# Performance work log

Measured on AMD Instinct MI355X. Metric: run time of the kernel, lower is better.

Reference implementation:

```python
import jax, jax.numpy as jnp
import numpy as np


def _conv2d_valid(x, w):
    # x: (N, C, H, W), w: (O, C, kH, kW) -> (N, O, H-kH+1, W-kW+1)
    return jax.lax.conv_general_dilated(
        x, w, window_strides=(1, 1), padding='VALID',
        dimension_numbers=('NCHW', 'OIHW', 'NCHW'))


def setup_inputs() -> dict:
    key = jax.random.key(0)
    kx, ky = jax.random.split(key)
    x = jax.random.normal(kx, (16, 64, 128, 128), dtype=jnp.float32)
    y = jax.random.normal(ky, (64, 64, 16, 16), dtype=jnp.float32)
    return {"x": x, "y": y}


def reference(x, y):
    # Normalize each of the K kernels to unit L2 norm (sum over C, kH, kW).
    normed_y = y / jnp.sqrt(jnp.sum(y * y, axis=(1, 2, 3), keepdims=True))
    # Per-window L2 norm of x via ones-kernel box conv over x^2.
    ones_kernel = jnp.ones(y.shape, dtype=x.dtype)
    x_norm = jnp.sqrt(_conv2d_valid(x * x, ones_kernel))
    # Normalized cross-correlation, clamped at zero.
    diss = _conv2d_valid(x, normed_y) / x_norm
    return jax.nn.relu(diss)
```

## Files before the change

kernel.cpp:

```cpp
#include <hip/hip_runtime.h>
#include <stdint.h>

#define GAS __attribute__((address_space(1)))
#define LAS __attribute__((address_space(3)))

typedef __attribute__((ext_vector_type(8))) short short8;
typedef __attribute__((ext_vector_type(4))) float float4v;
typedef __attribute__((ext_vector_type(4))) unsigned int uint4v;

__device__ __forceinline__ unsigned short f2bf(float f) {
  union { float f; unsigned int u; } v; v.f = f;
  unsigned int r = v.u + 0x7fffu + ((v.u >> 16) & 1u);
  return (unsigned short)(r >> 16);
}

__device__ __forceinline__ void async_g2l16(const void* g, void* l) {
  __builtin_amdgcn_global_load_lds((const GAS unsigned int*)g,
                                   (LAS unsigned int*)l, 16, 0, 0);
}

__global__ void knorm_y(const float* __restrict__ y, unsigned short* __restrict__ y_t) {
  int o = blockIdx.x;
  int tid = threadIdx.x;
  const float* yo = y + o * 16384;
  float s = 0.f;
  for (int idx = tid; idx < 16384; idx += 256) { float v = yo[idx]; s += v * v; }
  for (int off = 32; off; off >>= 1) s += __shfl_down(s, off, 64);
  __shared__ float red[4];
  if ((tid & 63) == 0) red[tid >> 6] = s;
  __syncthreads();
  float rn = 1.0f / sqrtf(red[0] + red[1] + red[2] + red[3]);
  for (int idx = tid; idx < 16384; idx += 256) {
    int c = idx >> 8, dy = (idx >> 4) & 15, dx = idx & 15;
    unsigned short b = f2bf(yo[idx] * rn);
    int dst = ((dy * 16 + dx) * 64 + o) * 64 + (((c >> 3) ^ (o & 7)) << 3) + (c & 7);
    y_t[dst] = b;
  }
}

__global__ void ktrans_x(const float* __restrict__ x, unsigned short* __restrict__ x_t,
                         float* __restrict__ s) {
  int h = blockIdx.x, n = blockIdx.y;
  int tid = threadIdx.x;
  __shared__ __align__(16) unsigned short tb[8192];
  __shared__ float sb[256];
  const float* xb = x + ((size_t)n * 64) * 16384 + h * 128;
  for (int idx = tid; idx < 8192; idx += 256) {
    int c = idx >> 7, w = idx & 127;
    float v = xb[(size_t)c * 16384 + w];
    tb[w * 64 + (((c >> 3) ^ (w & 7)) << 3) + (c & 7)] = f2bf(v);
  }
  int w = tid & 127, half = tid >> 7;
  float acc = 0.f;
  for (int c = half * 32; c < half * 32 + 32; ++c) {
    float v = xb[(size_t)c * 16384 + w];
    acc += v * v;
  }
  sb[tid] = acc;
  __syncthreads();
  uint4v* dst = (uint4v*)(x_t + ((size_t)(n * 128 + h)) * 8192);
  const uint4v* src = (const uint4v*)tb;
  for (int idx = tid; idx < 1024; idx += 256) dst[idx] = src[idx];
  if (tid < 128) s[((size_t)(n * 128 + h)) * 128 + tid] = sb[tid] + sb[tid + 128];
}

__global__ void knorm_x(const float* __restrict__ s, float* __restrict__ invn) {
  int idx = blockIdx.x * 256 + threadIdx.x;
  if (idx >= 16 * 113 * 113) return;
  int n = idx / 12769, r = idx % 12769;
  int i = r / 113, j = r % 113;
  const float* sp = s + ((size_t)n * 128 + i) * 128 + j;
  float acc = 0.f;
#pragma unroll
  for (int dy = 0; dy < 16; ++dy) {
    float rowacc = 0.f;
#pragma unroll
    for (int dx = 0; dx < 16; ++dx) rowacc += sp[dy * 128 + dx];
    acc += rowacc;
  }
  invn[idx] = 1.0f / sqrtf(acc);
}

__launch_bounds__(256, 2)
__global__ void kconv(const unsigned short* __restrict__ x_t,
                      const unsigned short* __restrict__ y_t,
                      const float* __restrict__ invn,
                      float* __restrict__ out) {
  int i = blockIdx.x;
  int n = blockIdx.y;
  int tid = threadIdx.x;
  int lane = tid & 63, wave = tid >> 6;
  int lane15 = lane & 15, q = lane >> 4;
  int wrow = wave >> 1, wcol = wave & 1;

  __shared__ __align__(16) char smem[49152];
  char* const A0 = smem;
  char* const A1 = smem + 16384;
  char* const B0 = smem + 32768;
  char* const B1 = smem + 40960;

  const char* xrow0 = (const char*)(x_t + ((size_t)(n * 128 + i)) * 8192);

  auto stageA = [&](int dy, char* buf) {
    const char* src = xrow0 + (size_t)dy * 16384;
#pragma unroll
    for (int it = 0; it < 4; ++it) {
      int chunk = it * 256 + wave * 64;
      async_g2l16(src + (chunk + lane) * 16, buf + chunk * 16);
    }
  };
  auto stageB = [&](int t, char* buf) {
    const char* src = (const char*)(y_t + (size_t)t * 4096);
#pragma unroll
    for (int it = 0; it < 2; ++it) {
      int chunk = it * 256 + wave * 64;
      async_g2l16(src + (chunk + lane) * 16, buf + chunk * 16);
    }
  };

  float4v acc[4][2];
#pragma unroll
  for (int mt = 0; mt < 4; ++mt)
#pragma unroll
    for (int nt = 0; nt < 2; ++nt) acc[mt][nt] = (float4v){0.f, 0.f, 0.f, 0.f};

  int boff[2][2];
#pragma unroll
  for (int nt = 0; nt < 2; ++nt)
#pragma unroll
    for (int cb = 0; cb < 2; ++cb) {
      int o = wcol * 32 + nt * 16 + lane15;
      boff[nt][cb] = o * 128 + (((q + cb * 4) ^ (o & 7)) << 4);
    }
  int abase[4];
#pragma unroll
  for (int mt = 0; mt < 4; ++mt) abase[mt] = (wrow * 64 + mt * 16 + lane15) * 128;

  stageB(0, B0);
  stageA(0, A0);
  __syncthreads();

#pragma unroll 1
  for (int t = 0; t < 256; ++t) {
    int dx = t & 15, dy = t >> 4;
    if (t < 255) {
      stageB(t + 1, (t & 1) ? B0 : B1);
      if (((t + 1) & 15) == 0) stageA((t + 1) >> 4, ((((t + 1) >> 4) & 1) ? A1 : A0));
    }
    char* Ab = (dy & 1) ? A1 : A0;
    char* Bb = (t & 1) ? B1 : B0;

    short8 bf[2][2];
#pragma unroll
    for (int nt = 0; nt < 2; ++nt)
#pragma unroll
      for (int cb = 0; cb < 2; ++cb) bf[nt][cb] = *(const short8*)(Bb + boff[nt][cb]);

    int xr = (lane15 + dx) & 7;
#pragma unroll
    for (int cb = 0; cb < 2; ++cb) {
      int aoff = dx * 128 + ((((q + cb * 4) ^ xr)) << 4);
#pragma unroll
      for (int mt = 0; mt < 4; ++mt) {
        short8 a = *(const short8*)(Ab + abase[mt] + aoff);
        acc[mt][0] = __builtin_amdgcn_mfma_f32_16x16x32_bf16(a, bf[0][cb], acc[mt][0], 0, 0, 0);
        acc[mt][1] = __builtin_amdgcn_mfma_f32_16x16x32_bf16(a, bf[1][cb], acc[mt][1], 0, 0, 0);
      }
    }
    __syncthreads();
  }

  float* cs = (float*)smem;
#pragma unroll
  for (int mt = 0; mt < 4; ++mt)
#pragma unroll
    for (int nt = 0; nt < 2; ++nt) {
      int o = wcol * 32 + nt * 16 + lane15;
      int j0 = wrow * 64 + mt * 16 + q * 4;
      *(float4v*)(cs + o * 132 + j0) = acc[mt][nt];
    }
  __syncthreads();
  const float* ivp = invn + ((size_t)n * 113 + i) * 113;
  float* op = out + (size_t)n * 64 * 12769 + (size_t)i * 113;
  for (int idx = tid; idx < 8192; idx += 256) {
    int o = idx >> 7, j = idx & 127;
    if (j < 113) {
      float v = cs[o * 132 + j] * ivp[j];
      op[(size_t)o * 12769 + j] = fmaxf(v, 0.f);
    }
  }
}

extern "C" void kernel_launch(void* const* d_in, const int* in_sizes, int n_in,
                              void* d_out, int out_size, void* d_ws, size_t ws_size,
                              hipStream_t stream) {
  const float* x = (const float*)d_in[0];
  const float* y = (const float*)d_in[1];
  float* out = (float*)d_out;
  char* ws = (char*)d_ws;
  unsigned short* x_t = (unsigned short*)ws;
  unsigned short* y_t = (unsigned short*)(ws + 33554432);
  float* s = (float*)(ws + 35651584);
  float* invn = (float*)(ws + 36700160);

  hipLaunchKernelGGL(knorm_y, dim3(64), dim3(256), 0, stream, y, y_t);
  hipLaunchKernelGGL(ktrans_x, dim3(128, 16), dim3(256), 0, stream, x, x_t, s);
  hipLaunchKernelGGL(knorm_x, dim3(799), dim3(256), 0, stream, s, invn);
  hipLaunchKernelGGL(kconv, dim3(113, 16), dim3(256), 0, stream, x_t, y_t, invn, out);
}
```

Before: 598.8 us.

## Load conv filter fragments directly to registers, drop B LDS staging

The filter tensor is re-laid out so each lane can load its MFMA B fragments straight from global memory into registers. This removes the per-tap LDS staging and the barrier after every tap, leaving one barrier per filter row. LDS use drops to 32KB, so occupancy rises to 3 blocks per CU, and the epilogue is split into two halves to fit. The x transpose is fused with the sum-of-squares pass, and the window norm becomes a separable box sum. The cost is more global/L2 traffic for the filter, with one register double buffer hiding its latency.

```diff
diff --git a/kernel.cpp b/kernel.cpp
--- a/kernel.cpp
+++ b/kernel.cpp
@@ -19,7 +19,11 @@
                                    (LAS unsigned int*)l, 16, 0, 0);
 }
 
-__global__ void knorm_y(const float* __restrict__ y, unsigned short* __restrict__ y_t) {
+__device__ __forceinline__ void vmem_drain() {
+  asm volatile("s_waitcnt vmcnt(0)" ::: "memory");
+}
+
+__global__ void knorm_y(const float* __restrict__ y, unsigned short* __restrict__ y_t2) {
   int o = blockIdx.x;
   int tid = threadIdx.x;
   const float* yo = y + o * 16384;
@@ -30,11 +34,13 @@
   if ((tid & 63) == 0) red[tid >> 6] = s;
   __syncthreads();
   float rn = 1.0f / sqrtf(red[0] + red[1] + red[2] + red[3]);
+  int og = o >> 4, ol = o & 15;
   for (int idx = tid; idx < 16384; idx += 256) {
     int c = idx >> 8, dy = (idx >> 4) & 15, dx = idx & 15;
-    unsigned short b = f2bf(yo[idx] * rn);
-    int dst = ((dy * 16 + dx) * 64 + o) * 64 + (((c >> 3) ^ (o & 7)) << 3) + (c & 7);
-    y_t[dst] = b;
+    int t = dy * 16 + dx;
+    int cb = c >> 5, q = (c >> 3) & 3, j = c & 7;
+    size_t dst = (size_t)t * 4096 + (size_t)(og * 2 + cb) * 512 + (q * 16 + ol) * 8 + j;
+    y_t2[dst] = f2bf(yo[idx] * rn);
   }
 }
 
@@ -45,16 +51,20 @@
   __shared__ __align__(16) unsigned short tb[8192];
   __shared__ float sb[256];
   const float* xb = x + ((size_t)n * 64) * 16384 + h * 128;
-  for (int idx = tid; idx < 8192; idx += 256) {
-    int c = idx >> 7, w = idx & 127;
-    float v = xb[(size_t)c * 16384 + w];
-    tb[w * 64 + (((c >> 3) ^ (w & 7)) << 3) + (c & 7)] = f2bf(v);
-  }
   int w = tid & 127, half = tid >> 7;
   float acc = 0.f;
-  for (int c = half * 32; c < half * 32 + 32; ++c) {
-    float v = xb[(size_t)c * 16384 + w];
-    acc += v * v;
+#pragma unroll
+  for (int cs = 0; cs < 4; ++cs) {
+    short8 tmp;
+#pragma unroll
+    for (int j = 0; j < 8; ++j) {
+      int c = half * 32 + cs * 8 + j;
+      float v = xb[(size_t)c * 16384 + w];
+      tmp[j] = (short)f2bf(v);
+      acc += v * v;
+    }
+    int chunk = (half * 4 + cs) ^ (w & 7);
+    *(short8*)(tb + w * 64 + chunk * 8) = tmp;
   }
   sb[tid] = acc;
   __syncthreads();
@@ -65,25 +75,26 @@
 }
 
 __global__ void knorm_x(const float* __restrict__ s, float* __restrict__ invn) {
-  int idx = blockIdx.x * 256 + threadIdx.x;
-  if (idx >= 16 * 113 * 113) return;
-  int n = idx / 12769, r = idx % 12769;
-  int i = r / 113, j = r % 113;
-  const float* sp = s + ((size_t)n * 128 + i) * 128 + j;
-  float acc = 0.f;
-#pragma unroll
-  for (int dy = 0; dy < 16; ++dy) {
-    float rowacc = 0.f;
-#pragma unroll
-    for (int dx = 0; dx < 16; ++dx) rowacc += sp[dy * 128 + dx];
-    acc += rowacc;
-  }
-  invn[idx] = 1.0f / sqrtf(acc);
-}
-
-__launch_bounds__(256, 2)
+  int i = blockIdx.x, n = blockIdx.y;
+  int tid = threadIdx.x;
+  __shared__ float colsum[128];
+  const float* sp = s + ((size_t)(n * 128 + i)) * 128;
+  float a = 0.f;
+#pragma unroll
+  for (int dy = 0; dy < 16; ++dy) a += sp[dy * 128 + tid];
+  colsum[tid] = a;
+  __syncthreads();
+  if (tid < 113) {
+    float acc = 0.f;
+#pragma unroll
+    for (int dx = 0; dx < 16; ++dx) acc += colsum[tid + dx];
+    invn[((size_t)n * 113 + i) * 113 + tid] = 1.0f / sqrtf(acc);
+  }
+}
+
+__launch_bounds__(256, 3)
 __global__ void kconv(const unsigned short* __restrict__ x_t,
-                      const unsigned short* __restrict__ y_t,
+                      const unsigned short* __restrict__ y_t2,
                       const float* __restrict__ invn,
                       float* __restrict__ out) {
   int i = blockIdx.x;
@@ -93,11 +104,9 @@
   int lane15 = lane & 15, q = lane >> 4;
   int wrow = wave >> 1, wcol = wave & 1;
 
-  __shared__ __align__(16) char smem[49152];
+  __shared__ __align__(16) char smem[32768];
   char* const A0 = smem;
   char* const A1 = smem + 16384;
-  char* const B0 = smem + 32768;
-  char* const B1 = smem + 40960;
 
   const char* xrow0 = (const char*)(x_t + ((size_t)(n * 128 + i)) * 8192);
 
@@ -109,13 +118,14 @@
       async_g2l16(src + (chunk + lane) * 16, buf + chunk * 16);
     }
   };
-  auto stageB = [&](int t, char* buf) {
-    const char* src = (const char*)(y_t + (size_t)t * 4096);
-#pragma unroll
-    for (int it = 0; it < 2; ++it) {
-      int chunk = it * 256 + wave * 64;
-      async_g2l16(src + (chunk + lane) * 16, buf + chunk * 16);
-    }
+
+  const short8* ybase = (const short8*)(y_t2 + (size_t)wcol * 2048 + (size_t)lane * 8);
+  auto loadB = [&](int t, short8 bf[2][2]) {
+    const short8* p = ybase + (size_t)t * 512;
+    bf[0][0] = p[0];
+    bf[0][1] = p[64];
+    bf[1][0] = p[128];
+    bf[1][1] = p[192];
   };
 
   float4v acc[4][2];
@@ -124,70 +134,71 @@
 #pragma unroll
     for (int nt = 0; nt < 2; ++nt) acc[mt][nt] = (float4v){0.f, 0.f, 0.f, 0.f};
 
-  int boff[2][2];
-#pragma unroll
-  for (int nt = 0; nt < 2; ++nt)
-#pragma unroll
-    for (int cb = 0; cb < 2; ++cb) {
-      int o = wcol * 32 + nt * 16 + lane15;
-      boff[nt][cb] = o * 128 + (((q + cb * 4) ^ (o & 7)) << 4);
-    }
   int abase[4];
 #pragma unroll
   for (int mt = 0; mt < 4; ++mt) abase[mt] = (wrow * 64 + mt * 16 + lane15) * 128;
 
-  stageB(0, B0);
   stageA(0, A0);
+  short8 bc[2][2];
+  loadB(0, bc);
+  vmem_drain();
   __syncthreads();
 
 #pragma unroll 1
-  for (int t = 0; t < 256; ++t) {
-    int dx = t & 15, dy = t >> 4;
-    if (t < 255) {
-      stageB(t + 1, (t & 1) ? B0 : B1);
-      if (((t + 1) & 15) == 0) stageA((t + 1) >> 4, ((((t + 1) >> 4) & 1) ? A1 : A0));
-    }
+  for (int dy = 0; dy < 16; ++dy) {
     char* Ab = (dy & 1) ? A1 : A0;
-    char* Bb = (t & 1) ? B1 : B0;
-
-    short8 bf[2][2];
-#pragma unroll
-    for (int nt = 0; nt < 2; ++nt)
-#pragma unroll
-      for (int cb = 0; cb < 2; ++cb) bf[nt][cb] = *(const short8*)(Bb + boff[nt][cb]);
-
-    int xr = (lane15 + dx) & 7;
-#pragma unroll
-    for (int cb = 0; cb < 2; ++cb) {
-      int aoff = dx * 128 + ((((q + cb * 4) ^ xr)) << 4);
-#pragma unroll
-      for (int mt = 0; mt < 4; ++mt) {
-        short8 a = *(const short8*)(Ab + abase[mt] + aoff);
-        acc[mt][0] = __builtin_amdgcn_mfma_f32_16x16x32_bf16(a, bf[0][cb], acc[mt][0], 0, 0, 0);
-        acc[mt][1] = __builtin_amdgcn_mfma_f32_16x16x32_bf16(a, bf[1][cb], acc[mt][1], 0, 0, 0);
+    if (dy < 15) stageA(dy + 1, (dy & 1) ? A0 : A1);
+#pragma unroll
+    for (int dx = 0; dx < 16; ++dx) {
+      int t = dy * 16 + dx;
+      short8 bn[2][2];
+      if (t < 255) loadB(t + 1, bn);
+      int xr = (lane15 + dx) & 7;
+#pragma unroll
+      for (int cb = 0; cb < 2; ++cb) {
+        int aoff = dx * 128 + (((q + cb * 4) ^ xr) << 4);
+#pragma unroll
+        for (int mt = 0; mt < 4; ++mt) {
+          short8 a = *(const short8*)(Ab + abase[mt] + aoff);
+          acc[mt][0] = __builtin_amdgcn_mfma_f32_16x16x32_bf16(a, bc[0][cb], acc[mt][0], 0, 0, 0);
+          acc[mt][1] = __builtin_amdgcn_mfma_f32_16x16x32_bf16(a, bc[1][cb], acc[mt][1], 0, 0, 0);
+        }
       }
-    }
+      if (t < 255) {
+        bc[0][0] = bn[0][0]; bc[0][1] = bn[0][1];
+        bc[1][0] = bn[1][0]; bc[1][1] = bn[1][1];
+      }
+    }
+    vmem_drain();
     __syncthreads();
   }
 
   float* cs = (float*)smem;
-#pragma unroll
-  for (int mt = 0; mt < 4; ++mt)
-#pragma unroll
-    for (int nt = 0; nt < 2; ++nt) {
-      int o = wcol * 32 + nt * 16 + lane15;
-      int j0 = wrow * 64 + mt * 16 + q * 4;
-      *(float4v*)(cs + o * 132 + j0) = acc[mt][nt];
-    }
-  __syncthreads();
+  float* ivs = cs + 4352;
   const float* ivp = invn + ((size_t)n * 113 + i) * 113;
+  if (tid < 128) ivs[tid] = (tid < 113) ? ivp[tid] : 0.f;
   float* op = out + (size_t)n * 64 * 12769 + (size_t)i * 113;
-  for (int idx = tid; idx < 8192; idx += 256) {
-    int o = idx >> 7, j = idx & 127;
-    if (j < 113) {
-      float v = cs[o * 132 + j] * ivp[j];
-      op[(size_t)o * 12769 + j] = fmaxf(v, 0.f);
-    }
+#pragma unroll 1
+  for (int p = 0; p < 2; ++p) {
+    if (wcol == p) {
+#pragma unroll
+      for (int mt = 0; mt < 4; ++mt)
+#pragma unroll
+        for (int nt = 0; nt < 2; ++nt) {
+          int row = nt * 16 + lane15;
+          int j0 = wrow * 64 + mt * 16 + q * 4;
+          *(float4v*)(cs + row * 132 + j0) = acc[mt][nt];
+        }
+    }
+    __syncthreads();
+    for (int idx = tid; idx < 4096; idx += 256) {
+      int o2 = idx >> 7, j = idx & 127;
+      if (j < 113) {
+        float v = cs[o2 * 132 + j] * ivs[j];
+        op[(size_t)(p * 32 + o2) * 12769 + j] = fmaxf(v, 0.f);
+      }
+    }
+    __syncthreads();
   }
 }
 
@@ -199,12 +210,12 @@
   float* out = (float*)d_out;
   char* ws = (char*)d_ws;
   unsigned short* x_t = (unsigned short*)ws;
-  unsigned short* y_t = (unsigned short*)(ws + 33554432);
+  unsigned short* y_t2 = (unsigned short*)(ws + 33554432);
   float* s = (float*)(ws + 35651584);
   float* invn = (float*)(ws + 36700160);
 
-  hipLaunchKernelGGL(knorm_y, dim3(64), dim3(256), 0, stream, y, y_t);
+  hipLaunchKernelGGL(knorm_y, dim3(64), dim3(256), 0, stream, y, y_t2);
   hipLaunchKernelGGL(ktrans_x, dim3(128, 16), dim3(256), 0, stream, x, x_t, s);
-  hipLaunchKernelGGL(knorm_x, dim3(799), dim3(256), 0, stream, s, invn);
-  hipLaunchKernelGGL(kconv, dim3(113, 16), dim3(256), 0, stream, x_t, y_t, invn, out);
-}
+  hipLaunchKernelGGL(knorm_x, dim3(113, 16), dim3(128), 0, stream, s, invn);
+  hipLaunchKernelGGL(kconv, dim3(113, 16), dim3(256), 0, stream, x_t, y_t2, invn, out);
+}
```

Result: faster. 546.5 us (-8.7%).
